# Kernel tuning notes

Measured on AMD Instinct MI355X. Metric: run time of the kernel, lower is better.

Reference implementation:

```python
import jax, jax.numpy as jnp
import numpy as np
import math

B, S, C = 8, 4096, 512
WIN = 16          # window_size
G = 4             # num_global_tokens
KS = 7            # conv kernel_size
CG = C // 4       # global proj dim


def setup_inputs() -> dict:
    key = jax.random.key(0)
    ks = jax.random.split(key, 16)
    s = 1.0 / math.sqrt(C)
    sg = 1.0 / math.sqrt(CG)
    return {
        "x": jax.random.normal(ks[0], (B, S, C), dtype=jnp.float32),
        "Wq": jax.random.normal(ks[1], (C, C), dtype=jnp.float32) * s,
        "bq": jnp.zeros((C,), dtype=jnp.float32),
        "Wk": jax.random.normal(ks[2], (C, C), dtype=jnp.float32) * s,
        "bk": jnp.zeros((C,), dtype=jnp.float32),
        "Wv": jax.random.normal(ks[3], (C, C), dtype=jnp.float32) * s,
        "bv": jnp.zeros((C,), dtype=jnp.float32),
        "Wo": jax.random.normal(ks[4], (C, C), dtype=jnp.float32) * s,
        "bo": jnp.zeros((C,), dtype=jnp.float32),
        "Wg": jax.random.normal(ks[5], (C, CG), dtype=jnp.float32) * s,
        "bg": jnp.zeros((CG,), dtype=jnp.float32),
        "Wgo": jax.random.normal(ks[6], (CG, C), dtype=jnp.float32) * sg,
        "bgo": jnp.zeros((C,), dtype=jnp.float32),
        "conv_w": jax.random.normal(ks[7], (1, 2, KS), dtype=jnp.float32) * 0.2,
    }


def _forward(x, Wq, bq, Wk, bk, Wv, bv, Wo, bo, Wg, bg, Wgo, bgo, conv_w):
    b, s, c = x.shape
    q = x @ Wq + bq
    k = x @ Wk + bk
    v = x @ Wv + bv

    nw = s // WIN
    qw = q.reshape(b, nw, WIN, c)
    kw = k.reshape(b, nw, WIN, c)
    vw = v.reshape(b, nw, WIN, c)
    scale = 1.0 / math.sqrt(c)
    attn = jax.nn.softmax(jnp.einsum('bnic,bnjc->bnij', qw, kw) * scale, axis=-1)
    x_local = jnp.einsum('bnij,bnjc->bnic', attn, vw).reshape(b, s, c)

    # ---- sparse global-token attention ----
    gidx = np.linspace(0, s - 1, G).astype(np.int64)  # static indices
    gt = x[:, gidx]                       # [B,G,C]
    qg = q @ Wg + bg                      # [B,S,CG]
    kg = gt @ Wg + bg                     # [B,G,CG]
    vg = kg
    gscale = 1.0 / math.sqrt(c // 4)
    gattn = jax.nn.softmax(jnp.einsum('bsd,bgd->bsg', qg, kg) * gscale, axis=-1)
    x_global = jnp.einsum('bsg,bgd->bsd', gattn, vg) @ Wgo + bgo  # [B,S,C]

    # ---- conv gate over channel-avg / channel-max ----
    avg = jnp.mean(x, axis=2, keepdims=True)          # [B,S,1]
    mx = jnp.max(x, axis=2, keepdims=True)            # [B,S,1]
    pool = jnp.concatenate([avg, mx], axis=2)         # [B,S,2]
    pool = jnp.transpose(pool, (0, 2, 1))             # [B,2,S]
    gate = jax.lax.conv_general_dilated(
        pool, conv_w, window_strides=(1,), padding=[(KS // 2, KS // 2)],
        dimension_numbers=('NCH', 'OIH', 'NCH'))      # [B,1,S]
    gate = jax.nn.sigmoid(jnp.transpose(gate, (0, 2, 1)))  # [B,S,1]

    out = (x + x_local + x_global) * gate
    return out @ Wo + bo


def reference(x, Wq, bq, Wk, bk, Wv, bv, Wo, bo, Wg, bg, Wgo, bgo, conv_w):
    return _forward(x, Wq, bq, Wk, bk, Wv, bv, Wo, bo, Wg, bg, Wgo, bgo, conv_w)
```

## Files before the change

kernel.cpp:

```cpp
#include <hip/hip_runtime.h>
#include <hip/hip_bf16.h>

#define BB 8
#define SS 4096
#define CC 512
#define NTOK (BB*SS)
#define QKVS 1664

typedef __attribute__((ext_vector_type(8))) short bf16x8;
typedef __attribute__((ext_vector_type(4))) float f32x4;
typedef __attribute__((ext_vector_type(4))) short s16x4;

__device__ __forceinline__ float bf2f(short s) {
  return __uint_as_float(((unsigned)(unsigned short)s) << 16);
}
__device__ __forceinline__ short f2bf(float f) {
  __hip_bfloat16 h = __float2bfloat16(f);
  return *reinterpret_cast<short*>(&h);
}

__device__ __forceinline__ f32x4 pv_mfma(s16x4 a, s16x4 b, f32x4 c) {
#if __has_builtin(__builtin_amdgcn_mfma_f32_16x16x16bf16_1k)
  return __builtin_amdgcn_mfma_f32_16x16x16bf16_1k(a, b, c, 0, 0, 0);
#else
  f32x4 d;
  asm volatile("v_mfma_f32_16x16x16_bf16 %0, %1, %2, %3\n\ts_nop 7\n\ts_nop 7"
               : "=v"(d) : "v"(a), "v"(b), "v"(c));
  return d;
#endif
}

__device__ __forceinline__ void gload_lds16(const short* g, short* l) {
  __builtin_amdgcn_global_load_lds(
      (const __attribute__((address_space(1))) unsigned int*)g,
      (__attribute__((address_space(3))) unsigned int*)l, 16, 0, 0);
}

__global__ __launch_bounds__(256) void prep_weights(
    const float* __restrict__ Wq, const float* __restrict__ Wk, const float* __restrict__ Wv,
    const float* __restrict__ Wo, const float* __restrict__ Wg,
    const float* __restrict__ bq, const float* __restrict__ bk, const float* __restrict__ bv,
    const float* __restrict__ bg,
    short* __restrict__ WtQKV, short* __restrict__ WtO, short* __restrict__ WtG,
    short* __restrict__ Wqb, float* __restrict__ bqkv, float* __restrict__ zb)
{
  int i = blockIdx.x * 256 + threadIdx.x;
  if (i < 1536 * 512) {
    int n = i >> 9, k = i & 511;
    const float* W = (n < 512) ? Wq : (n < 1024) ? Wk : Wv;
    WtQKV[i] = f2bf(W[k * 512 + (n & 511)]);
  }
  if (i < 512 * 512) {
    int n = i >> 9, k = i & 511;
    WtO[i] = f2bf(Wo[k * 512 + n]);
    Wqb[i] = f2bf(Wq[i]);
  }
  if (i < 128 * 512) {
    int n = i >> 9, k = i & 511;
    WtG[i] = f2bf(Wg[k * 128 + n]);
  }
  if (i < 1536) {
    bqkv[i] = (i < 512) ? bq[i] : (i < 1024) ? bk[i - 512] : bv[i - 1024];
  }
  if (i < 512) zb[i] = 0.f;
  if (i < 128) {
    float s = bg[i];
    for (int c = 0; c < 512; c++) s += bq[c] * Wg[c * 128 + i];
    bqkv[1536 + i] = s;
  }
}

__global__ __launch_bounds__(256) void cast_pool_kernel(const float* __restrict__ x,
                                                        short* __restrict__ xb,
                                                        float* __restrict__ pavg,
                                                        float* __restrict__ pmax)
{
  int tok = blockIdx.x * 4 + (threadIdx.x >> 6);
  int lane = threadIdx.x & 63;
  const float* xr = &x[(size_t)tok * CC];
  float4 a = *(const float4*)&xr[lane * 4];
  float4 b = *(const float4*)&xr[256 + lane * 4];
  s16x4 oa, ob;
  oa[0] = f2bf(a.x); oa[1] = f2bf(a.y); oa[2] = f2bf(a.z); oa[3] = f2bf(a.w);
  ob[0] = f2bf(b.x); ob[1] = f2bf(b.y); ob[2] = f2bf(b.z); ob[3] = f2bf(b.w);
  *(s16x4*)&xb[(size_t)tok * CC + lane * 4] = oa;
  *(s16x4*)&xb[(size_t)tok * CC + 256 + lane * 4] = ob;
  float s = (a.x + a.y) + (a.z + a.w) + (b.x + b.y) + (b.z + b.w);
  float m = fmaxf(fmaxf(fmaxf(a.x, a.y), fmaxf(a.z, a.w)),
                  fmaxf(fmaxf(b.x, b.y), fmaxf(b.z, b.w)));
#pragma unroll
  for (int off = 32; off; off >>= 1) {
    s += __shfl_down(s, off);
    m = fmaxf(m, __shfl_down(m, off));
  }
  if (lane == 0) { pavg[tok] = s * (1.0f / CC); pmax[tok] = m; }
}

template<int OUT_BF16, int SWZ>
__global__ __launch_bounds__(256, 3) void gemm_kernel(
    const short* __restrict__ A,
    const short* __restrict__ Wt,
    const float* __restrict__ bias,
    void* __restrict__ Cp, int ldc, int nx)
{
  __shared__ short As[128 * 64];
  __shared__ short Bs[128 * 64];
  int id = blockIdx.x;
  if (SWZ) {
    const int cpx = gridDim.x >> 3;
    id = (id & 7) * cpx + (id >> 3);
  }
  const int n0 = (id % nx) * 128;
  const int m0 = (id / nx) * 128;
  const int t = threadIdx.x;
  const int lane = t & 63, w = t >> 6;
  const int wm = (w >> 1) * 64, wn = (w & 1) * 64;
  const int lr = lane & 15;
  const int g8b = (lane >> 4) * 16;
  const int xorb = (lr & 7) << 4;

  const int srow = w * 8 + (lane >> 3);
  const int scol = (((lane & 7) ^ (lane >> 3)) << 4) >> 1;
  const short* Ag = A + (size_t)(m0 + srow) * 512 + scol;
  const short* Bg = Wt + (size_t)(n0 + srow) * 512 + scol;
  short* Al = &As[(w * 8) * 64];
  short* Bl = &Bs[(w * 8) * 64];

  f32x4 acc[4][4];
#pragma unroll
  for (int i = 0; i < 4; i++)
#pragma unroll
    for (int j = 0; j < 4; j++) acc[i][j] = (f32x4){0.f, 0.f, 0.f, 0.f};

  for (int k0 = 0; k0 < 512; k0 += 64) {
#pragma unroll
    for (int s = 0; s < 4; s++) {
      gload_lds16(Ag + k0 + s * (32 * 512), Al + s * (32 * 64));
      gload_lds16(Bg + k0 + s * (32 * 512), Bl + s * (32 * 64));
    }
    __syncthreads();
#pragma unroll
    for (int kk = 0; kk < 2; kk++) {
      bf16x8 af[4], bfr[4];
      const int ko = ((kk * 64 + g8b) ^ xorb) >> 1;
#pragma unroll
      for (int mt = 0; mt < 4; mt++) af[mt]  = *(bf16x8*)&As[(wm + mt * 16 + lr) * 64 + ko];
#pragma unroll
      for (int nt = 0; nt < 4; nt++) bfr[nt] = *(bf16x8*)&Bs[(wn + nt * 16 + lr) * 64 + ko];
#pragma unroll
      for (int mt = 0; mt < 4; mt++)
#pragma unroll
        for (int nt = 0; nt < 4; nt++)
          acc[mt][nt] = __builtin_amdgcn_mfma_f32_16x16x32_bf16(af[mt], bfr[nt], acc[mt][nt], 0, 0, 0);
    }
    __syncthreads();
  }

  const int cr = (lane >> 4) * 4;
#pragma unroll
  for (int nt = 0; nt < 4; nt++) {
    int col = n0 + wn + nt * 16 + lr;
    float bv = bias[col];
#pragma unroll
    for (int mt = 0; mt < 4; mt++) {
      int row = m0 + wm + mt * 16 + cr;
#pragma unroll
      for (int j = 0; j < 4; j++) {
        float v = acc[mt][nt][j] + bv;
        if (OUT_BF16) ((short*)Cp)[(size_t)(row + j) * ldc + col] = f2bf(v);
        else          ((float*)Cp)[(size_t)(row + j) * ldc + col] = v;
      }
    }
  }
}

__global__ __launch_bounds__(256, 4) void winattn_combine_kernel(
    const short* __restrict__ qkvb, const short* __restrict__ xb,
    const float* __restrict__ kg, const float* __restrict__ kgo,
    const float* __restrict__ bgo, const float* __restrict__ pavg,
    const float* __restrict__ pmax, const float* __restrict__ conv_w,
    short* __restrict__ y)
{
  __shared__ short xls[32][528];
  __shared__ float scs[32][4];
  __shared__ float4 esm[32];
  __shared__ float gateb[32];
  const int t = threadIdx.x;
  const int t0b = blockIdx.x * 32;
  const int bb = t0b >> 12;

  if (t < 128) {
    const int tl = t >> 2, gi = t & 3;
    const short* qr = &qkvb[(size_t)(t0b + tl) * QKVS + 1536];
    const float* kr = &kg[bb * 512 + gi * 128];
    float s = 0.f;
    for (int d0 = 0; d0 < 128; d0 += 8) {
      bf16x8 qv = *(const bf16x8*)&qr[d0];
#pragma unroll
      for (int u = 0; u < 8; u++) s += bf2f(qv[u]) * kr[d0 + u];
    }
    scs[tl][gi] = s * 0.08838834764831845f;
  }
  __syncthreads();
  if (t < 32) {
    float p0 = scs[t][0], p1 = scs[t][1], p2 = scs[t][2], p3 = scs[t][3];
    float mx = fmaxf(fmaxf(p0, p1), fmaxf(p2, p3));
    float e0 = __expf(p0 - mx), e1 = __expf(p1 - mx), e2 = __expf(p2 - mx), e3 = __expf(p3 - mx);
    float inv = 1.0f / (e0 + e1 + e2 + e3);
    esm[t] = make_float4(e0 * inv, e1 * inv, e2 * inv, e3 * inv);
    int s = (t0b + t) & 4095;
    float g = 0.f;
#pragma unroll
    for (int tk = 0; tk < 7; tk++) {
      int ss = s + tk - 3;
      if (ss >= 0 && ss < SS)
        g += conv_w[tk] * pavg[bb * SS + ss] + conv_w[7 + tk] * pmax[bb * SS + ss];
    }
    gateb[t] = 1.0f / (1.0f + __expf(-g));
  }

  const int lane = t & 63, w = t >> 6;
  const int t0 = t0b + (w >> 1) * 16;
  const int half = w & 1;
  const int qrow = lane & 15;
  const int grp8 = (lane >> 4) * 8;
  const int krow = (lane >> 4) * 4;
  const int colo = lane & 15;

  const short* kqbase = &qkvb[(size_t)(t0 + qrow) * QKVS];
  f32x4 accA = (f32x4){0.f, 0.f, 0.f, 0.f};
  f32x4 accB = (f32x4){0.f, 0.f, 0.f, 0.f};
#pragma unroll
  for (int k0 = 0; k0 < 512; k0 += 64) {
    bf16x8 kf0 = *(const bf16x8*)&kqbase[512 + k0 + grp8];
    bf16x8 qf0 = *(const bf16x8*)&kqbase[k0 + grp8];
    bf16x8 kf1 = *(const bf16x8*)&kqbase[512 + k0 + 32 + grp8];
    bf16x8 qf1 = *(const bf16x8*)&kqbase[k0 + 32 + grp8];
    accA = __builtin_amdgcn_mfma_f32_16x16x32_bf16(kf0, qf0, accA, 0, 0, 0);
    accB = __builtin_amdgcn_mfma_f32_16x16x32_bf16(kf1, qf1, accB, 0, 0, 0);
  }

  const short* vbase = &qkvb[(size_t)t0 * QKVS + 1024];
  s16x4 vreg[16];
#pragma unroll
  for (int ct = 0; ct < 16; ct++) {
    const int c0 = half * 256 + ct * 16 + colo;
#pragma unroll
    for (int u = 0; u < 4; u++)
      vreg[ct][u] = vbase[(size_t)(krow + u) * QKVS + c0];
  }

  const float scale = 0.04419417382415922f;
  float s0 = (accA[0] + accB[0]) * scale, s1 = (accA[1] + accB[1]) * scale;
  float s2 = (accA[2] + accB[2]) * scale, s3 = (accA[3] + accB[3]) * scale;
  float m = fmaxf(fmaxf(s0, s1), fmaxf(s2, s3));
  m = fmaxf(m, __shfl_xor(m, 16));
  m = fmaxf(m, __shfl_xor(m, 32));
  float e0 = __expf(s0 - m), e1 = __expf(s1 - m), e2 = __expf(s2 - m), e3 = __expf(s3 - m);
  float sum = e0 + e1 + e2 + e3;
  sum += __shfl_xor(sum, 16);
  sum += __shfl_xor(sum, 32);
  float inv = 1.0f / sum;
  s16x4 pa;
  pa[0] = f2bf(e0 * inv); pa[1] = f2bf(e1 * inv);
  pa[2] = f2bf(e2 * inv); pa[3] = f2bf(e3 * inv);

  const int rbase = (w >> 1) * 16 + krow;
#pragma unroll
  for (int ct = 0; ct < 16; ct++) {
    const int c0 = half * 256 + ct * 16 + colo;
    f32x4 d = pv_mfma(pa, vreg[ct], (f32x4){0.f, 0.f, 0.f, 0.f});
#pragma unroll
    for (int jj = 0; jj < 4; jj++)
      xls[rbase + jj][c0] = f2bf(d[jj]);
  }
  __syncthreads();

  const int r = t >> 3;
  const int rowg = t0b + r;
  const float4 e = esm[r];
  const float g = gateb[r];
  const float* kgr = &kgo[bb * 2048];
  const short* xrow = &xb[(size_t)rowg * CC];
  short* yrow = &y[(size_t)rowg * CC];
#pragma unroll
  for (int it = 0; it < 8; it++) {
    const int c = (t & 7) * 8 + it * 64;
    bf16x8 xv  = *(const bf16x8*)&xrow[c];
    bf16x8 xlv = *(const bf16x8*)&xls[r][c];
    float4 k0a = *(const float4*)&kgr[c],        k0b = *(const float4*)&kgr[c + 4];
    float4 k1a = *(const float4*)&kgr[512 + c],  k1b = *(const float4*)&kgr[512 + c + 4];
    float4 k2a = *(const float4*)&kgr[1024 + c], k2b = *(const float4*)&kgr[1024 + c + 4];
    float4 k3a = *(const float4*)&kgr[1536 + c], k3b = *(const float4*)&kgr[1536 + c + 4];
    float4 ba  = *(const float4*)&bgo[c],        bbv = *(const float4*)&bgo[c + 4];
    float xg[8];
    xg[0] = e.x * k0a.x + e.y * k1a.x + e.z * k2a.x + e.w * k3a.x + ba.x;
    xg[1] = e.x * k0a.y + e.y * k1a.y + e.z * k2a.y + e.w * k3a.y + ba.y;
    xg[2] = e.x * k0a.z + e.y * k1a.z + e.z * k2a.z + e.w * k3a.z + ba.z;
    xg[3] = e.x * k0a.w + e.y * k1a.w + e.z * k2a.w + e.w * k3a.w + ba.w;
    xg[4] = e.x * k0b.x + e.y * k1b.x + e.z * k2b.x + e.w * k3b.x + bbv.x;
    xg[5] = e.x * k0b.y + e.y * k1b.y + e.z * k2b.y + e.w * k3b.y + bbv.y;
    xg[6] = e.x * k0b.z + e.y * k1b.z + e.z * k2b.z + e.w * k3b.z + bbv.z;
    xg[7] = e.x * k0b.w + e.y * k1b.w + e.z * k2b.w + e.w * k3b.w + bbv.w;
    bf16x8 ov;
#pragma unroll
    for (int u = 0; u < 8; u++)
      ov[u] = f2bf((bf2f(xv[u]) + bf2f(xlv[u]) + xg[u]) * g);
    *(bf16x8*)&yrow[c] = ov;
  }
}

__global__ __launch_bounds__(256) void kg_kgo_kernel(const float* __restrict__ x,
                                                     const float* __restrict__ Wg,
                                                     const float* __restrict__ bg,
                                                     const float* __restrict__ Wgo,
                                                     float* __restrict__ kg,
                                                     float* __restrict__ kgo)
{
  __shared__ float kr[128];
  const int bg_ = blockIdx.x;
  const int b = bg_ >> 2, g = bg_ & 3;
  const int gidx[4] = {0, 1365, 2730, 4095};
  const int t = threadIdx.x;
  const float* xr = &x[((size_t)b * SS + gidx[g]) * CC];
  if (t < 128) {
    float s = bg[t];
    for (int c = 0; c < CC; c++) s += xr[c] * Wg[c * 128 + t];
    kr[t] = s;
    kg[bg_ * 128 + t] = s;
  }
  __syncthreads();
  for (int c = t; c < 512; c += 256) {
    float s = 0.f;
    for (int d = 0; d < 128; d++) s += kr[d] * Wgo[d * 512 + c];
    kgo[bg_ * 512 + c] = s;
  }
}

extern "C" void kernel_launch(void* const* d_in, const int* in_sizes, int n_in,
                              void* d_out, int out_size, void* d_ws, size_t ws_size,
                              hipStream_t stream)
{
  const float* x     = (const float*)d_in[0];
  const float* Wq    = (const float*)d_in[1];
  const float* bq    = (const float*)d_in[2];
  const float* Wk    = (const float*)d_in[3];
  const float* bk    = (const float*)d_in[4];
  const float* Wv    = (const float*)d_in[5];
  const float* bv    = (const float*)d_in[6];
  const float* Wo    = (const float*)d_in[7];
  const float* bo    = (const float*)d_in[8];
  const float* Wg    = (const float*)d_in[9];
  const float* bg    = (const float*)d_in[10];
  const float* Wgo   = (const float*)d_in[11];
  const float* bgo   = (const float*)d_in[12];
  const float* convw = (const float*)d_in[13];
  float* out = (float*)d_out;

  char* ws = (char*)d_ws;
  size_t off = 0;
  auto alloc = [&](size_t bytes) -> void* {
    void* p = ws + off;
    off += (bytes + 255) & ~(size_t)255;
    return p;
  };
  short* xb    = (short*)alloc((size_t)NTOK * CC * 2);
  short* qkvb  = (short*)alloc((size_t)NTOK * QKVS * 2);
  short* WtQKV = (short*)alloc((size_t)QKVS * 512 * 2);
  short* WtO   = (short*)alloc((size_t)512 * 512 * 2);
  short* WtG   = (short*)alloc((size_t)128 * 512 * 2);
  short* Wqb   = (short*)alloc((size_t)512 * 512 * 2);
  float* bqkv  = (float*)alloc(QKVS * 4);
  float* zb    = (float*)alloc(512 * 4);
  float* kg    = (float*)alloc(8 * 4 * 128 * 4);
  float* kgo   = (float*)alloc(8 * 4 * 512 * 4);
  float* pavg  = (float*)alloc((size_t)NTOK * 4);
  float* pmax  = (float*)alloc((size_t)NTOK * 4);
  short* ybuf  = (short*)alloc((size_t)NTOK * CC * 2);
  short* WtQG  = WtQKV + (size_t)1536 * 512;

  prep_weights<<<3072, 256, 0, stream>>>(Wq, Wk, Wv, Wo, Wg, bq, bk, bv, bg,
                                         WtQKV, WtO, WtG, Wqb, bqkv, zb);
  cast_pool_kernel<<<NTOK / 4, 256, 0, stream>>>(x, xb, pavg, pmax);
  kg_kgo_kernel<<<32, 256, 0, stream>>>(x, Wg, bg, Wgo, kg, kgo);

  gemm_kernel<1, 0><<<4, 256, 0, stream>>>(WtG, Wqb, zb, WtQG, 512, 4);

  gemm_kernel<1, 1><<<13 * 256, 256, 0, stream>>>(xb, WtQKV, bqkv, qkvb, QKVS, 13);

  winattn_combine_kernel<<<NTOK / 32, 256, 0, stream>>>(qkvb, xb, kg, kgo, bgo,
                                                        pavg, pmax, convw, ybuf);

  gemm_kernel<0, 1><<<4 * 256, 256, 0, stream>>>(ybuf, WtO, bo, out, CC, 4);
}
```

Measured before the change: 217.1 us.

## Double-buffer GEMM LDS tiles and stage V through swizzled LDS in window attention

The GEMM now ping-pongs between two LDS buffers per operand. The global-to-LDS load of the next K slice is issued before the MFMAs on the current slice run, which needs only one barrier per stage, and launch bounds drop from 3 to 2 blocks to fit the doubled LDS. The window-attention kernel now loads V rows into XOR-swizzled LDS with asynchronous loads at kernel start. This replaces the strided per-element global gathers into registers. The P·V results are written back into that same LDS buffer in place of a separate xls array. The intent is to hide global latency and cut uncoalesced V reads, at the cost of lower GEMM occupancy.

```diff
diff --git a/kernel.cpp b/kernel.cpp
--- a/kernel.cpp
+++ b/kernel.cpp
@@ -97,14 +97,14 @@
 }
 
 template<int OUT_BF16, int SWZ>
-__global__ __launch_bounds__(256, 3) void gemm_kernel(
+__global__ __launch_bounds__(256, 2) void gemm_kernel(
     const short* __restrict__ A,
     const short* __restrict__ Wt,
     const float* __restrict__ bias,
     void* __restrict__ Cp, int ldc, int nx)
 {
-  __shared__ short As[128 * 64];
-  __shared__ short Bs[128 * 64];
+  __shared__ short As0[128 * 64], As1[128 * 64];
+  __shared__ short Bs0[128 * 64], Bs1[128 * 64];
   int id = blockIdx.x;
   if (SWZ) {
     const int cpx = gridDim.x >> 3;
@@ -123,8 +123,7 @@
   const int scol = (((lane & 7) ^ (lane >> 3)) << 4) >> 1;
   const short* Ag = A + (size_t)(m0 + srow) * 512 + scol;
   const short* Bg = Wt + (size_t)(n0 + srow) * 512 + scol;
-  short* Al = &As[(w * 8) * 64];
-  short* Bl = &Bs[(w * 8) * 64];
+  const int sloff = (w * 8) * 64;
 
   f32x4 acc[4][4];
 #pragma unroll
@@ -132,29 +131,50 @@
 #pragma unroll
     for (int j = 0; j < 4; j++) acc[i][j] = (f32x4){0.f, 0.f, 0.f, 0.f};
 
-  for (int k0 = 0; k0 < 512; k0 += 64) {
-#pragma unroll
-    for (int s = 0; s < 4; s++) {
-      gload_lds16(Ag + k0 + s * (32 * 512), Al + s * (32 * 64));
-      gload_lds16(Bg + k0 + s * (32 * 512), Bl + s * (32 * 64));
-    }
+#define STAGE(AL, BL, KOFF)                                          \
+  do {                                                               \
+    _Pragma("unroll")                                                \
+    for (int s_ = 0; s_ < 4; s_++) {                                 \
+      gload_lds16(Ag + (KOFF) + s_ * (32 * 512), &AL[sloff + s_ * (32 * 64)]); \
+      gload_lds16(Bg + (KOFF) + s_ * (32 * 512), &BL[sloff + s_ * (32 * 64)]); \
+    }                                                                \
+  } while (0)
+
+#define COMPUTE(AL, BL)                                                           \
+  do {                                                                            \
+    _Pragma("unroll")                                                             \
+    for (int kk = 0; kk < 2; kk++) {                                              \
+      bf16x8 af[4], bfr[4];                                                       \
+      const int ko = ((kk * 64 + g8b) ^ xorb) >> 1;                               \
+      _Pragma("unroll")                                                           \
+      for (int mt = 0; mt < 4; mt++) af[mt]  = *(bf16x8*)&AL[(wm + mt * 16 + lr) * 64 + ko]; \
+      _Pragma("unroll")                                                           \
+      for (int nt = 0; nt < 4; nt++) bfr[nt] = *(bf16x8*)&BL[(wn + nt * 16 + lr) * 64 + ko]; \
+      _Pragma("unroll")                                                           \
+      for (int mt = 0; mt < 4; mt++)                                              \
+        _Pragma("unroll")                                                         \
+        for (int nt = 0; nt < 4; nt++)                                            \
+          acc[mt][nt] = __builtin_amdgcn_mfma_f32_16x16x32_bf16(af[mt], bfr[nt], acc[mt][nt], 0, 0, 0); \
+    }                                                                             \
+  } while (0)
+
+  STAGE(As0, Bs0, 0);
+  __syncthreads();
+#pragma unroll
+  for (int tt = 0; tt < 3; tt++) {
+    STAGE(As1, Bs1, tt * 128 + 64);
+    COMPUTE(As0, Bs0);
     __syncthreads();
-#pragma unroll
-    for (int kk = 0; kk < 2; kk++) {
-      bf16x8 af[4], bfr[4];
-      const int ko = ((kk * 64 + g8b) ^ xorb) >> 1;
-#pragma unroll
-      for (int mt = 0; mt < 4; mt++) af[mt]  = *(bf16x8*)&As[(wm + mt * 16 + lr) * 64 + ko];
-#pragma unroll
-      for (int nt = 0; nt < 4; nt++) bfr[nt] = *(bf16x8*)&Bs[(wn + nt * 16 + lr) * 64 + ko];
-#pragma unroll
-      for (int mt = 0; mt < 4; mt++)
-#pragma unroll
-        for (int nt = 0; nt < 4; nt++)
-          acc[mt][nt] = __builtin_amdgcn_mfma_f32_16x16x32_bf16(af[mt], bfr[nt], acc[mt][nt], 0, 0, 0);
-    }
+    STAGE(As0, Bs0, tt * 128 + 128);
+    COMPUTE(As1, Bs1);
     __syncthreads();
   }
+  STAGE(As1, Bs1, 448);
+  COMPUTE(As0, Bs0);
+  __syncthreads();
+  COMPUTE(As1, Bs1);
+#undef STAGE
+#undef COMPUTE
 
   const int cr = (lane >> 4) * 4;
 #pragma unroll
@@ -181,13 +201,26 @@
     const float* __restrict__ pmax, const float* __restrict__ conv_w,
     short* __restrict__ y)
 {
-  __shared__ short xls[32][528];
+  __shared__ short vs[2][16][512];
   __shared__ float scs[32][4];
   __shared__ float4 esm[32];
   __shared__ float gateb[32];
   const int t = threadIdx.x;
+  const int lane = t & 63, w = t >> 6;
   const int t0b = blockIdx.x * 32;
   const int bb = t0b >> 12;
+  const int win = w >> 1, half = w & 1;
+  const int t0 = t0b + win * 16;
+
+  {
+    const int rb = half * 8;
+#pragma unroll
+    for (int i = 0; i < 8; i++) {
+      const int r = rb + i;
+      const short* vrow = &qkvb[(size_t)(t0 + r) * QKVS + 1024];
+      gload_lds16(vrow + ((lane ^ (r & 7)) << 3), &vs[win][r][0]);
+    }
+  }
 
   if (t < 128) {
     const int tl = t >> 2, gi = t & 3;
@@ -219,9 +252,6 @@
     gateb[t] = 1.0f / (1.0f + __expf(-g));
   }
 
-  const int lane = t & 63, w = t >> 6;
-  const int t0 = t0b + (w >> 1) * 16;
-  const int half = w & 1;
   const int qrow = lane & 15;
   const int grp8 = (lane >> 4) * 8;
   const int krow = (lane >> 4) * 4;
@@ -238,16 +268,6 @@
     bf16x8 qf1 = *(const bf16x8*)&kqbase[k0 + 32 + grp8];
     accA = __builtin_amdgcn_mfma_f32_16x16x32_bf16(kf0, qf0, accA, 0, 0, 0);
     accB = __builtin_amdgcn_mfma_f32_16x16x32_bf16(kf1, qf1, accB, 0, 0, 0);
-  }
-
-  const short* vbase = &qkvb[(size_t)t0 * QKVS + 1024];
-  s16x4 vreg[16];
-#pragma unroll
-  for (int ct = 0; ct < 16; ct++) {
-    const int c0 = half * 256 + ct * 16 + colo;
-#pragma unroll
-    for (int u = 0; u < 4; u++)
-      vreg[ct][u] = vbase[(size_t)(krow + u) * QKVS + c0];
   }
 
   const float scale = 0.04419417382415922f;
@@ -265,29 +285,38 @@
   pa[0] = f2bf(e0 * inv); pa[1] = f2bf(e1 * inv);
   pa[2] = f2bf(e2 * inv); pa[3] = f2bf(e3 * inv);
 
-  const int rbase = (w >> 1) * 16 + krow;
 #pragma unroll
   for (int ct = 0; ct < 16; ct++) {
-    const int c0 = half * 256 + ct * 16 + colo;
-    f32x4 d = pv_mfma(pa, vreg[ct], (f32x4){0.f, 0.f, 0.f, 0.f});
-#pragma unroll
-    for (int jj = 0; jj < 4; jj++)
-      xls[rbase + jj][c0] = f2bf(d[jj]);
+    const int cb = (half * 256 + ct * 16 + colo) * 2;
+    s16x4 bf;
+#pragma unroll
+    for (int u = 0; u < 4; u++) {
+      const int r = krow + u;
+      bf[u] = vs[win][r][(cb ^ ((r & 7) << 4)) >> 1];
+    }
+    f32x4 d = pv_mfma(pa, bf, (f32x4){0.f, 0.f, 0.f, 0.f});
+#pragma unroll
+    for (int jj = 0; jj < 4; jj++) {
+      const int r = krow + jj;
+      vs[win][r][(cb ^ ((r & 7) << 4)) >> 1] = f2bf(d[jj]);
+    }
   }
   __syncthreads();
 
   const int r = t >> 3;
   const int rowg = t0b + r;
+  const int winr = r >> 4, rr = r & 15;
   const float4 e = esm[r];
   const float g = gateb[r];
   const float* kgr = &kgo[bb * 2048];
   const short* xrow = &xb[(size_t)rowg * CC];
+  const short* xlrow = &vs[winr][rr][0];
   short* yrow = &y[(size_t)rowg * CC];
 #pragma unroll
   for (int it = 0; it < 8; it++) {
     const int c = (t & 7) * 8 + it * 64;
     bf16x8 xv  = *(const bf16x8*)&xrow[c];
-    bf16x8 xlv = *(const bf16x8*)&xls[r][c];
+    bf16x8 xlv = *(const bf16x8*)&xlrow[((c * 2) ^ ((rr & 7) << 4)) >> 1];
     float4 k0a = *(const float4*)&kgr[c],        k0b = *(const float4*)&kgr[c + 4];
     float4 k1a = *(const float4*)&kgr[512 + c],  k1b = *(const float4*)&kgr[512 + c + 4];
     float4 k2a = *(const float4*)&kgr[1024 + c], k2b = *(const float4*)&kgr[1024 + c + 4];
```

Measured after the change: 213.2 us. About the same (-1.8%).
